# Optimization experiments

Hardware: AMD Instinct MI355X
Metric: run time of the kernel (lower is better)

Reference implementation:

```python
import jax, jax.numpy as jnp
import numpy as np

NUM_CLASS = 80
S = 76              # output_size = 608 // 8 (scale i=0)
STRIDE = 8.0
XYSCALE = 1.2
IOU_LOSS_THRESH = 0.5
INPUT_SIZE = 608.0  # stride * output_size
ANCHORS0 = np.array([[12., 16.], [19., 36.], [40., 28.]], dtype=np.float32)


def setup_inputs() -> dict:
    key = jax.random.key(0)
    k1, k2, k3 = jax.random.split(key, 3)
    B, MAXGT = 16, 150
    conv = jax.random.normal(k1, (B, S, S, 3 * (5 + NUM_CLASS)), dtype=jnp.float32)
    label = jax.random.uniform(k2, (B, S, S, 3, 5 + NUM_CLASS), dtype=jnp.float32)
    # scale the xywh channels of label to pixel coordinates
    label = label.at[..., :4].multiply(INPUT_SIZE)
    bboxes = jax.random.uniform(k3, (B, MAXGT, 4), dtype=jnp.float32) * INPUT_SIZE
    return {"conv": conv, "label": label, "bboxes": bboxes}


def _bce_with_logits(logits, labels):
    # tf.nn.sigmoid_cross_entropy_with_logits, numerically stable form
    return jnp.maximum(logits, 0.0) - logits * labels + jnp.log1p(jnp.exp(-jnp.abs(logits)))


def _xywh_to_corners(b):
    return jnp.concatenate([b[..., :2] - b[..., 2:] * 0.5,
                            b[..., :2] + b[..., 2:] * 0.5], axis=-1)


def _bbox_iou(boxes1, boxes2):
    area1 = boxes1[..., 2] * boxes1[..., 3]
    area2 = boxes2[..., 2] * boxes2[..., 3]
    b1, b2 = _xywh_to_corners(boxes1), _xywh_to_corners(boxes2)
    lu = jnp.maximum(b1[..., :2], b2[..., :2])
    rd = jnp.minimum(b1[..., 2:], b2[..., 2:])
    inter = jnp.maximum(rd - lu, 0.0)
    inter_area = inter[..., 0] * inter[..., 1]
    union = area1 + area2 - inter_area
    return inter_area / union


def _bbox_giou(boxes1, boxes2):
    area1 = boxes1[..., 2] * boxes1[..., 3]
    area2 = boxes2[..., 2] * boxes2[..., 3]
    b1, b2 = _xywh_to_corners(boxes1), _xywh_to_corners(boxes2)
    lu = jnp.maximum(b1[..., :2], b2[..., :2])
    rd = jnp.minimum(b1[..., 2:], b2[..., 2:])
    inter = jnp.maximum(rd - lu, 0.0)
    inter_area = inter[..., 0] * inter[..., 1]
    union = area1 + area2 - inter_area
    iou = inter_area / union
    enc_lu = jnp.minimum(b1[..., :2], b2[..., :2])
    enc_rd = jnp.maximum(b1[..., 2:], b2[..., 2:])
    enc = jnp.maximum(enc_rd - enc_lu, 0.0)
    enc_area = enc[..., 0] * enc[..., 1]
    return iou - (enc_area - union) / enc_area


def _decode_train(conv):
    B = conv.shape[0]
    conv = conv.reshape(B, S, S, 3, 5 + NUM_CLASS)
    dxdy, dwdh, raw_conf, raw_prob = jnp.split(conv, [2, 4, 5], axis=-1)
    xs, ys = jnp.meshgrid(jnp.arange(S), jnp.arange(S))  # indexing='xy' like tf.meshgrid
    grid = jnp.stack([xs, ys], axis=-1)[None, :, :, None, :].astype(jnp.float32)  # [1,S,S,1,2]
    pred_xy = (jax.nn.sigmoid(dxdy) * XYSCALE - 0.5 * (XYSCALE - 1.0) + grid) * STRIDE
    pred_wh = jnp.exp(dwdh) * ANCHORS0  # [B,S,S,3,2]
    return jnp.concatenate([pred_xy, pred_wh,
                            jax.nn.sigmoid(raw_conf), jax.nn.sigmoid(raw_prob)], axis=-1)


def reference(conv, label, bboxes):
    pred = _decode_train(conv)  # [B,S,S,3,5+C]
    B = conv.shape[0]
    conv5 = conv.reshape(B, S, S, 3, 5 + NUM_CLASS)
    conv_raw_conf = conv5[..., 4:5]
    conv_raw_prob = conv5[..., 5:]

    pred_xywh = pred[..., 0:4]
    pred_conf = pred[..., 4:5]

    label_xywh = label[..., 0:4]
    respond_bbox = label[..., 4:5]
    label_prob = label[..., 5:]

    giou = _bbox_giou(pred_xywh, label_xywh)[..., None]
    bbox_loss_scale = 2.0 - label_xywh[..., 2:3] * label_xywh[..., 3:4] / (INPUT_SIZE ** 2)
    giou_loss = respond_bbox * bbox_loss_scale * (1.0 - giou)

    # pairwise IoU: [B,S,S,3,1,4] vs [B,1,1,1,MAXGT,4] -> [B,S,S,3,MAXGT]
    iou = _bbox_iou(pred_xywh[..., None, :], bboxes[:, None, None, None, :, :])
    max_iou = jnp.max(iou, axis=-1, keepdims=True)
    respond_bgd = (1.0 - respond_bbox) * (max_iou < IOU_LOSS_THRESH).astype(jnp.float32)

    conf_focal = jnp.square(respond_bbox - pred_conf)
    bce_conf = _bce_with_logits(conv_raw_conf, respond_bbox)
    conf_loss = conf_focal * (respond_bbox * bce_conf + respond_bgd * bce_conf)
    prob_loss = respond_bbox * _bce_with_logits(conv_raw_prob, label_prob)

    giou_loss = jnp.mean(jnp.sum(giou_loss, axis=(1, 2, 3, 4)))
    conf_loss = jnp.mean(jnp.sum(conf_loss, axis=(1, 2, 3, 4)))
    prob_loss = jnp.mean(jnp.sum(prob_loss, axis=(1, 2, 3, 4)))
    return jnp.stack([giou_loss, conf_loss, prob_loss])
```

## Files before the change

kernel.cpp:

```cpp
#include <hip/hip_runtime.h>
#include <math.h>

#define S 76
#define A 3
#define CH 85
#define MAXGT 150
#define CPB (S * S * A)
#define FPB (CPB * CH)
#define BATCH 16
#define TILE 64
#define BLK 256
#define N4F (TILE * CH / 4)
#define GX ((CPB + TILE - 1) / TILE)
#define NBLK (GX * BATCH)

__device__ __forceinline__ float frcp(float x) { return __builtin_amdgcn_rcpf(x); }
__device__ __forceinline__ float sigmoidf_(float x) { return frcp(1.f + __expf(-x)); }
__device__ __forceinline__ float bcef(float x, float y) {
    const float t  = __builtin_amdgcn_exp2f(x * 1.44269504f);
    const float lg = __builtin_amdgcn_logf(1.f + t);
    return __builtin_fmaf(0.69314718f, lg, -x * y);
}

__global__ __launch_bounds__(BLK) void yolo_unified_kernel(
    const float* __restrict__ conv, const float* __restrict__ label,
    const float* __restrict__ bboxes, float* __restrict__ part)
{
    __shared__ float  s_ch[TILE][5];
    __shared__ float  s_lh[TILE][5];
    __shared__ float  s_resp[TILE];
    __shared__ float4 s_box[MAXGT];
    __shared__ float  s_ba[MAXGT];
    __shared__ float  sred[3][BLK / 64];

    const int b   = blockIdx.y;
    const int tid = threadIdx.x;
    const int base_cell = blockIdx.x * TILE;
    const int ncells = min(TILE, CPB - base_cell);
    const int n4 = (ncells * CH) >> 2;

    const size_t eb = (size_t)b * FPB + (size_t)base_cell * CH;
    const float*  lbb = label + eb;
    const float4* cv4 = (const float4*)(conv + eb);
    const float4* lb4 = (const float4*)lbb;

    if (tid < MAXGT) {
        const float4 bx = *(const float4*)(bboxes + (size_t)b * (MAXGT * 4) + tid * 4);
        const float hw = bx.z * 0.5f, hh = bx.w * 0.5f;
        s_box[tid] = make_float4(3.f * (bx.x - hw), bx.y - hh, 3.f * (bx.x + hw), bx.y + hh);
        s_ba[tid]  = bx.z * bx.w;
    }
    if (tid < TILE)
        s_resp[tid] = (tid < ncells) ? lbb[(size_t)tid * CH + 4] : 0.f;
    __syncthreads();

    float p_sum = 0.f;
    auto body = [&](int u) {
        const float4 cc = cv4[u];
        const float4 lc = lb4[u];
        const unsigned e0 = 4u * (unsigned)u;
        const unsigned c0 = e0 / 85u;
        const unsigned r0 = e0 - 85u * c0;
        const float rsp = s_resp[c0];
        const float cx[4] = {cc.x, cc.y, cc.z, cc.w};
        const float lx[4] = {lc.x, lc.y, lc.z, lc.w};
        float s = 0.f;
        #pragma unroll
        for (int k = 0; k < 4; ++k) {
            const unsigned rr = r0 + (unsigned)k;
            const float bv = bcef(cx[k], lx[k]);
            s += ((rr - 5u) < 80u) ? bv : 0.f;
            const bool hdr = (rr < 5u) || (rr >= 85u);
            if (hdr) {
                const unsigned cell = (rr < 5u) ? c0 : c0 + 1u;
                const unsigned chn  = (rr < 5u) ? rr : rr - 85u;
                s_ch[cell][chn] = cx[k];
                s_lh[cell][chn] = lx[k];
            }
        }
        p_sum = __builtin_fmaf(rsp, s, p_sum);
    };
    if (n4 == N4F) {
        #pragma unroll
        for (int r = 0; r < N4F / BLK; ++r) body(r * BLK + tid);
        if (tid < (N4F - (N4F / BLK) * BLK)) body((N4F / BLK) * BLK + tid);
    } else {
        for (int u = tid; u < n4; u += BLK) body(u);
    }
    __syncthreads();

    const int c = tid >> 2;
    const int q = tid & 3;
    float g_sum = 0.f, c_sum = 0.f;
    if (c < ncells) {
        const int t   = base_cell + c;
        const int i   = t / (S * A);
        const int rem = t - i * (S * A);
        const int j   = rem / A;
        const int a   = rem - j * A;
        const float aw = (a == 0) ? 12.f : ((a == 1) ? 19.f : 40.f);
        const float ah = (a == 0) ? 16.f : ((a == 1) ? 36.f : 28.f);

        const float dx = s_ch[c][0], dy = s_ch[c][1], dw = s_ch[c][2],
                    dh = s_ch[c][3], rc = s_ch[c][4];
        const float lxc = s_lh[c][0], lyc = s_lh[c][1], lwc = s_lh[c][2],
                    lhc = s_lh[c][3], resp = s_lh[c][4];

        const float px = (sigmoidf_(dx) * 1.2f - 0.1f + (float)j) * 8.f;
        const float py = (sigmoidf_(dy) * 1.2f - 0.1f + (float)i) * 8.f;
        const float pw = __expf(dw) * aw;
        const float ph = __expf(dh) * ah;
        const float pconf = sigmoidf_(rc);

        const float px1 = px - pw * 0.5f, py1 = py - ph * 0.5f;
        const float px2 = px + pw * 0.5f, py2 = py + ph * 0.5f;
        const float areap = pw * ph;

        const float px1_3 = 3.f * px1, px2_3 = 3.f * px2;
        float maxv = -1e30f;
        #pragma unroll 5
        for (int k = q; k < MAXGT; k += 4) {
            const float4 bx = s_box[k];
            const float ba  = s_ba[k];
            const float kiw3 = fmaxf(fminf(px2_3, bx.z) - fmaxf(px1_3, bx.x), 0.f);
            const float kih  = fmaxf(fminf(py2, bx.w) - fmaxf(py1, bx.y), 0.f);
            maxv = fmaxf(maxv, __builtin_fmaf(kiw3, kih, -ba));
        }
        maxv = fmaxf(maxv, __shfl_xor(maxv, 1, 64));
        maxv = fmaxf(maxv, __shfl_xor(maxv, 2, 64));

        if (q == 0) {
            const float lx1 = lxc - lwc * 0.5f, ly1 = lyc - lhc * 0.5f;
            const float lx2 = lxc + lwc * 0.5f, ly2 = lyc + lhc * 0.5f;
            const float areal = lwc * lhc;
            const float iw = fmaxf(fminf(px2, lx2) - fmaxf(px1, lx1), 0.f);
            const float ih = fmaxf(fminf(py2, ly2) - fmaxf(py1, ly1), 0.f);
            const float inter = iw * ih;
            const float uni = areap + areal - inter;
            const float iou = inter * frcp(uni);
            const float ew = fmaxf(fmaxf(px2, lx2) - fminf(px1, lx1), 0.f);
            const float eh = fmaxf(fmaxf(py2, ly2) - fminf(py1, ly1), 0.f);
            const float enc = ew * eh;
            const float giou = iou - (enc - uni) * frcp(enc);
            g_sum = resp * (2.f - areal * (1.f / (608.f * 608.f))) * (1.f - giou);

            const float bgd = (1.f - resp) * ((maxv < areap) ? 1.f : 0.f);
            const float focal = (resp - pconf) * (resp - pconf);
            c_sum = focal * (resp + bgd) * bcef(rc, resp);
        }
    }

    for (int off = 32; off > 0; off >>= 1) {
        g_sum += __shfl_down(g_sum, off, 64);
        c_sum += __shfl_down(c_sum, off, 64);
        p_sum += __shfl_down(p_sum, off, 64);
    }
    const int lane = tid & 63, wv = tid >> 6;
    if (lane == 0) { sred[0][wv] = g_sum; sred[1][wv] = c_sum; sred[2][wv] = p_sum; }
    __syncthreads();
    if (tid == 0) {
        float G = 0.f, C = 0.f, P = 0.f;
        #pragma unroll
        for (int w = 0; w < BLK / 64; ++w) { G += sred[0][w]; C += sred[1][w]; P += sred[2][w]; }
        const int bid = blockIdx.y * gridDim.x + blockIdx.x;
        part[bid * 3 + 0] = G;
        part[bid * 3 + 1] = C;
        part[bid * 3 + 2] = P;
    }
}

__global__ __launch_bounds__(256) void final_reduce(
    const float* __restrict__ part, float* __restrict__ out, int nblocks, float invB)
{
    const int tid = threadIdx.x;
    float g = 0.f, c = 0.f, p = 0.f;
    for (int k = tid; k < nblocks; k += 256) {
        g += part[3 * k + 0];
        c += part[3 * k + 1];
        p += part[3 * k + 2];
    }
    for (int off = 32; off > 0; off >>= 1) {
        g += __shfl_down(g, off, 64);
        c += __shfl_down(c, off, 64);
        p += __shfl_down(p, off, 64);
    }
    __shared__ float sred[3][4];
    const int lane = tid & 63, wv = tid >> 6;
    if (lane == 0) { sred[0][wv] = g; sred[1][wv] = c; sred[2][wv] = p; }
    __syncthreads();
    if (tid == 0) {
        float G = 0.f, C = 0.f, P = 0.f;
        #pragma unroll
        for (int w = 0; w < 4; ++w) { G += sred[0][w]; C += sred[1][w]; P += sred[2][w]; }
        out[0] = G * invB;
        out[1] = C * invB;
        out[2] = P * invB;
    }
}

extern "C" void kernel_launch(void* const* d_in, const int* in_sizes, int n_in,
                              void* d_out, int out_size, void* d_ws, size_t ws_size,
                              hipStream_t stream) {
    const float* conv   = (const float*)d_in[0];
    const float* label  = (const float*)d_in[1];
    const float* bboxes = (const float*)d_in[2];
    float* out  = (float*)d_out;
    float* part = (float*)d_ws;

    dim3 grid(GX, BATCH);
    yolo_unified_kernel<<<grid, BLK, 0, stream>>>(conv, label, bboxes, part);
    final_reduce<<<1, 256, 0, stream>>>(part, out, NBLK, 1.f / (float)BATCH);
}
```

Before: 63.72 us.

## Stream tiles via async global-to-LDS ring buffer with larger per-block tiles

Tiles grow from 64 to 192 cells per block. On full tiles, each wave streams its contiguous slice of conv and label through a 4-deep LDS ring using global_load_lds, with explicit vmcnt waits, to overlap memory latency with the BCE math. The max-IoU scan now runs one thread per cell over all 150 boxes instead of four threads per cell plus shuffles. This trades fewer blocks and a serial IoU loop per thread for better latency hiding, and relies on hand-tuned waitcnt ordering that may be fragile.

```diff
diff --git a/kernel.cpp b/kernel.cpp
--- a/kernel.cpp
+++ b/kernel.cpp
@@ -8,11 +8,16 @@
 #define CPB (S * S * A)
 #define FPB (CPB * CH)
 #define BATCH 16
-#define TILE 64
 #define BLK 256
-#define N4F (TILE * CH / 4)
+#define WPB 4
+#define TILE 192
+#define F4_W 1020
+#define ROUNDS 16
+#define DEPTH 4
 #define GX ((CPB + TILE - 1) / TILE)
 #define NBLK (GX * BATCH)
+
+typedef float fx4 __attribute__((ext_vector_type(4)));
 
 __device__ __forceinline__ float frcp(float x) { return __builtin_amdgcn_rcpf(x); }
 __device__ __forceinline__ float sigmoidf_(float x) { return frcp(1.f + __expf(-x)); }
@@ -22,95 +27,163 @@
     return __builtin_fmaf(0.69314718f, lg, -x * y);
 }
 
+template<int N>
+__device__ __forceinline__ void vmwait() {
+    asm volatile("s_waitcnt vmcnt(%0)" :: "i"(N) : "memory");
+    __builtin_amdgcn_sched_barrier(0);
+}
+__device__ __forceinline__ void gl_lds16(const float* g, void* l) {
+    __builtin_amdgcn_global_load_lds(
+        (const __attribute__((address_space(1))) void*)g,
+        (__attribute__((address_space(3))) void*)l, 16, 0, 0);
+}
+
 __global__ __launch_bounds__(BLK) void yolo_unified_kernel(
     const float* __restrict__ conv, const float* __restrict__ label,
     const float* __restrict__ bboxes, float* __restrict__ part)
 {
-    __shared__ float  s_ch[TILE][5];
-    __shared__ float  s_lh[TILE][5];
-    __shared__ float  s_resp[TILE];
-    __shared__ float4 s_box[MAXGT];
-    __shared__ float  s_ba[MAXGT];
-    __shared__ float  sred[3][BLK / 64];
-
-    const int b   = blockIdx.y;
-    const int tid = threadIdx.x;
-    const int base_cell = blockIdx.x * TILE;
+    __shared__ fx4   ring_c[WPB * DEPTH * 64];
+    __shared__ fx4   ring_l[WPB * DEPTH * 64];
+    __shared__ float s_ch[TILE][5];
+    __shared__ float s_lh[TILE][5];
+    __shared__ float s_resp[TILE];
+    __shared__ fx4   s_box[MAXGT];
+    __shared__ float s_ba[MAXGT];
+    __shared__ float sred[3][WPB];
+
+    const int b    = blockIdx.y;
+    const int tile = blockIdx.x;
+    const int tid  = threadIdx.x;
+    const int w    = tid >> 6;
+    const int lane = tid & 63;
+    const int base_cell = tile * TILE;
     const int ncells = min(TILE, CPB - base_cell);
-    const int n4 = (ncells * CH) >> 2;
 
     const size_t eb = (size_t)b * FPB + (size_t)base_cell * CH;
-    const float*  lbb = label + eb;
-    const float4* cv4 = (const float4*)(conv + eb);
-    const float4* lb4 = (const float4*)lbb;
+    const float* cvb = conv  + eb;
+    const float* lbb = label + eb;
 
     if (tid < MAXGT) {
         const float4 bx = *(const float4*)(bboxes + (size_t)b * (MAXGT * 4) + tid * 4);
         const float hw = bx.z * 0.5f, hh = bx.w * 0.5f;
-        s_box[tid] = make_float4(3.f * (bx.x - hw), bx.y - hh, 3.f * (bx.x + hw), bx.y + hh);
+        fx4 v; v.x = 3.f * (bx.x - hw); v.y = bx.y - hh;
+        v.z = 3.f * (bx.x + hw); v.w = bx.y + hh;
+        s_box[tid] = v;
         s_ba[tid]  = bx.z * bx.w;
     }
-    if (tid < TILE)
-        s_resp[tid] = (tid < ncells) ? lbb[(size_t)tid * CH + 4] : 0.f;
+    for (int c = tid; c < ncells; c += BLK)
+        s_resp[c] = lbb[(size_t)c * CH + 4];
     __syncthreads();
 
     float p_sum = 0.f;
-    auto body = [&](int u) {
-        const float4 cc = cv4[u];
-        const float4 lc = lb4[u];
-        const unsigned e0 = 4u * (unsigned)u;
-        const unsigned c0 = e0 / 85u;
-        const unsigned r0 = e0 - 85u * c0;
-        const float rsp = s_resp[c0];
-        const float cx[4] = {cc.x, cc.y, cc.z, cc.w};
-        const float lx[4] = {lc.x, lc.y, lc.z, lc.w};
-        float s = 0.f;
-        #pragma unroll
-        for (int k = 0; k < 4; ++k) {
-            const unsigned rr = r0 + (unsigned)k;
-            const float bv = bcef(cx[k], lx[k]);
-            s += ((rr - 5u) < 80u) ? bv : 0.f;
-            const bool hdr = (rr < 5u) || (rr >= 85u);
-            if (hdr) {
-                const unsigned cell = (rr < 5u) ? c0 : c0 + 1u;
-                const unsigned chn  = (rr < 5u) ? rr : rr - 85u;
-                s_ch[cell][chn] = cx[k];
-                s_lh[cell][chn] = lx[k];
+
+    if (ncells == TILE) {
+        const float* pc = cvb + ((size_t)w * F4_W + (size_t)lane) * 4;
+        const float* pl = lbb + ((size_t)w * F4_W + (size_t)lane) * 4;
+
+        #define SLOT(R) ((w * DEPTH + ((R) & 3)) * 64)
+        #define ISSUE(R)                                                       \
+            gl_lds16(pc + (size_t)(R) * 256, &ring_c[SLOT(R)]);                \
+            gl_lds16(pl + (size_t)(R) * 256, &ring_l[SLOT(R)]);
+
+        ISSUE(0) ISSUE(1) ISSUE(2) ISSUE(3)
+        fx4 rc[2], rl[2];
+        vmwait<6>();
+        rc[0] = ring_c[SLOT(0) + lane];
+        rl[0] = ring_l[SLOT(0) + lane];
+        __builtin_amdgcn_sched_barrier(0);
+
+        #define STEPX(R, W_)                                                    \
+        {                                                                       \
+            if ((R) + 1 < ROUNDS) {                                             \
+                vmwait<W_>();                                                   \
+                rc[((R) + 1) & 1] = ring_c[SLOT((R) + 1) + lane];               \
+                rl[((R) + 1) & 1] = ring_l[SLOT((R) + 1) + lane];               \
+                __builtin_amdgcn_sched_barrier(0);                              \
+            }                                                                   \
+            if ((R) < ROUNDS - 1 || lane < 60) {                                \
+                const fx4 cc = rc[(R) & 1];                                     \
+                const fx4 lc = rl[(R) & 1];                                     \
+                const unsigned e0 = 4u * (unsigned)(w * F4_W + (R) * 64 + lane);\
+                const unsigned c0 = e0 / 85u;                                   \
+                const unsigned r0 = e0 - 85u * c0;                              \
+                const float rsp = s_resp[c0];                                   \
+                const float cxx[4] = {cc.x, cc.y, cc.z, cc.w};                  \
+                const float lxx[4] = {lc.x, lc.y, lc.z, lc.w};                  \
+                float s_ = 0.f;                                                 \
+                _Pragma("unroll")                                               \
+                for (int k = 0; k < 4; ++k) {                                   \
+                    const unsigned rr = r0 + (unsigned)k;           \
+                    const float bv = bcef(cxx[k], lxx[k]);                      \
+                    s_ += ((rr - 5u) < 80u) ? bv : 0.f;                         \
+                    if (rr < 5u)       { s_ch[c0][rr] = cxx[k];                 \
+                                         s_lh[c0][rr] = lxx[k]; }               \
+                    else if (rr >= 85u){ s_ch[c0 + 1][rr - 85u] = cxx[k];       \
+                                         s_lh[c0 + 1][rr - 85u] = lxx[k]; }     \
+                }                                                               \
+                p_sum = __builtin_fmaf(rsp, s_, p_sum);                         \
+            }                                                                   \
+            if ((R) < ROUNDS - 1) {                                             \
+                asm volatile("s_waitcnt lgkmcnt(0)" ::: "memory");              \
+                __builtin_amdgcn_sched_barrier(0);                              \
+                if ((R) + DEPTH < ROUNDS) { ISSUE((R) + DEPTH) }                \
+            }                                                                   \
+        }
+        STEPX(0, 4)  STEPX(1, 4)  STEPX(2, 4)  STEPX(3, 4)
+        STEPX(4, 4)  STEPX(5, 4)  STEPX(6, 4)  STEPX(7, 4)
+        STEPX(8, 4)  STEPX(9, 4)  STEPX(10, 4) STEPX(11, 4)
+        STEPX(12, 4) STEPX(13, 2) STEPX(14, 0) STEPX(15, 0)
+        #undef STEPX
+        #undef ISSUE
+        #undef SLOT
+    } else {
+        const int n4 = (ncells * CH) >> 2;
+        const fx4* cv4 = (const fx4*)cvb;
+        const fx4* lb4 = (const fx4*)lbb;
+        for (int u = tid; u < n4; u += BLK) {
+            const fx4 cc = cv4[u];
+            const fx4 lc = lb4[u];
+            const unsigned e0 = 4u * (unsigned)u;
+            const unsigned c0 = e0 / 85u;
+            const unsigned r0 = e0 - 85u * c0;
+            const float rsp = s_resp[c0];
+            const float cxx[4] = {cc.x, cc.y, cc.z, cc.w};
+            const float lxx[4] = {lc.x, lc.y, lc.z, lc.w};
+            float s_ = 0.f;
+            #pragma unroll
+            for (int k = 0; k < 4; ++k) {
+                const unsigned rr = r0 + (unsigned)k;
+                const float bv = bcef(cxx[k], lxx[k]);
+                s_ += ((rr - 5u) < 80u) ? bv : 0.f;
+                if (rr < 5u)        { s_ch[c0][rr] = cxx[k];  s_lh[c0][rr] = lxx[k]; }
+                else if (rr >= 85u) { s_ch[c0 + 1][rr - 85u] = cxx[k];
+                                      s_lh[c0 + 1][rr - 85u] = lxx[k]; }
             }
+            p_sum = __builtin_fmaf(rsp, s_, p_sum);
         }
-        p_sum = __builtin_fmaf(rsp, s, p_sum);
-    };
-    if (n4 == N4F) {
-        #pragma unroll
-        for (int r = 0; r < N4F / BLK; ++r) body(r * BLK + tid);
-        if (tid < (N4F - (N4F / BLK) * BLK)) body((N4F / BLK) * BLK + tid);
-    } else {
-        for (int u = tid; u < n4; u += BLK) body(u);
-    }
-    __syncthreads();
-
-    const int c = tid >> 2;
-    const int q = tid & 3;
+    }
+    __syncthreads();
+
     float g_sum = 0.f, c_sum = 0.f;
-    if (c < ncells) {
-        const int t   = base_cell + c;
-        const int i   = t / (S * A);
-        const int rem = t - i * (S * A);
+    if (tid < ncells) {
+        const int t_  = base_cell + tid;
+        const int i   = t_ / (S * A);
+        const int rem = t_ - i * (S * A);
         const int j   = rem / A;
         const int a   = rem - j * A;
         const float aw = (a == 0) ? 12.f : ((a == 1) ? 19.f : 40.f);
         const float ah = (a == 0) ? 16.f : ((a == 1) ? 36.f : 28.f);
 
-        const float dx = s_ch[c][0], dy = s_ch[c][1], dw = s_ch[c][2],
-                    dh = s_ch[c][3], rc = s_ch[c][4];
-        const float lxc = s_lh[c][0], lyc = s_lh[c][1], lwc = s_lh[c][2],
-                    lhc = s_lh[c][3], resp = s_lh[c][4];
+        const float dx = s_ch[tid][0], dy = s_ch[tid][1], dw = s_ch[tid][2],
+                    dh = s_ch[tid][3], rcv = s_ch[tid][4];
+        const float lxc = s_lh[tid][0], lyc = s_lh[tid][1], lwc = s_lh[tid][2],
+                    lhc = s_lh[tid][3], resp = s_lh[tid][4];
 
         const float px = (sigmoidf_(dx) * 1.2f - 0.1f + (float)j) * 8.f;
         const float py = (sigmoidf_(dy) * 1.2f - 0.1f + (float)i) * 8.f;
         const float pw = __expf(dw) * aw;
         const float ph = __expf(dh) * ah;
-        const float pconf = sigmoidf_(rc);
+        const float pconf = sigmoidf_(rcv);
 
         const float px1 = px - pw * 0.5f, py1 = py - ph * 0.5f;
         const float px2 = px + pw * 0.5f, py2 = py + ph * 0.5f;
@@ -119,35 +192,31 @@
         const float px1_3 = 3.f * px1, px2_3 = 3.f * px2;
         float maxv = -1e30f;
         #pragma unroll 5
-        for (int k = q; k < MAXGT; k += 4) {
-            const float4 bx = s_box[k];
+        for (int k = 0; k < MAXGT; ++k) {
+            const fx4 bx = s_box[k];
             const float ba  = s_ba[k];
             const float kiw3 = fmaxf(fminf(px2_3, bx.z) - fmaxf(px1_3, bx.x), 0.f);
             const float kih  = fmaxf(fminf(py2, bx.w) - fmaxf(py1, bx.y), 0.f);
             maxv = fmaxf(maxv, __builtin_fmaf(kiw3, kih, -ba));
         }
-        maxv = fmaxf(maxv, __shfl_xor(maxv, 1, 64));
-        maxv = fmaxf(maxv, __shfl_xor(maxv, 2, 64));
-
-        if (q == 0) {
-            const float lx1 = lxc - lwc * 0.5f, ly1 = lyc - lhc * 0.5f;
-            const float lx2 = lxc + lwc * 0.5f, ly2 = lyc + lhc * 0.5f;
-            const float areal = lwc * lhc;
-            const float iw = fmaxf(fminf(px2, lx2) - fmaxf(px1, lx1), 0.f);
-            const float ih = fmaxf(fminf(py2, ly2) - fmaxf(py1, ly1), 0.f);
-            const float inter = iw * ih;
-            const float uni = areap + areal - inter;
-            const float iou = inter * frcp(uni);
-            const float ew = fmaxf(fmaxf(px2, lx2) - fminf(px1, lx1), 0.f);
-            const float eh = fmaxf(fmaxf(py2, ly2) - fminf(py1, ly1), 0.f);
-            const float enc = ew * eh;
-            const float giou = iou - (enc - uni) * frcp(enc);
-            g_sum = resp * (2.f - areal * (1.f / (608.f * 608.f))) * (1.f - giou);
-
-            const float bgd = (1.f - resp) * ((maxv < areap) ? 1.f : 0.f);
-            const float focal = (resp - pconf) * (resp - pconf);
-            c_sum = focal * (resp + bgd) * bcef(rc, resp);
-        }
+
+        const float lx1 = lxc - lwc * 0.5f, ly1 = lyc - lhc * 0.5f;
+        const float lx2 = lxc + lwc * 0.5f, ly2 = lyc + lhc * 0.5f;
+        const float areal = lwc * lhc;
+        const float iw = fmaxf(fminf(px2, lx2) - fmaxf(px1, lx1), 0.f);
+        const float ih = fmaxf(fminf(py2, ly2) - fmaxf(py1, ly1), 0.f);
+        const float inter = iw * ih;
+        const float uni = areap + areal - inter;
+        const float iou = inter * frcp(uni);
+        const float ew = fmaxf(fmaxf(px2, lx2) - fminf(px1, lx1), 0.f);
+        const float eh = fmaxf(fmaxf(py2, ly2) - fminf(py1, ly1), 0.f);
+        const float enc = ew * eh;
+        const float giou = iou - (enc - uni) * frcp(enc);
+        g_sum = resp * (2.f - areal * (1.f / (608.f * 608.f))) * (1.f - giou);
+
+        const float bgd = (1.f - resp) * ((maxv < areap) ? 1.f : 0.f);
+        const float focal = (resp - pconf) * (resp - pconf);
+        c_sum = focal * (resp + bgd) * bcef(rcv, resp);
     }
 
     for (int off = 32; off > 0; off >>= 1) {
@@ -155,13 +224,12 @@
         c_sum += __shfl_down(c_sum, off, 64);
         p_sum += __shfl_down(p_sum, off, 64);
     }
-    const int lane = tid & 63, wv = tid >> 6;
-    if (lane == 0) { sred[0][wv] = g_sum; sred[1][wv] = c_sum; sred[2][wv] = p_sum; }
+    if (lane == 0) { sred[0][w] = g_sum; sred[1][w] = c_sum; sred[2][w] = p_sum; }
     __syncthreads();
     if (tid == 0) {
         float G = 0.f, C = 0.f, P = 0.f;
         #pragma unroll
-        for (int w = 0; w < BLK / 64; ++w) { G += sred[0][w]; C += sred[1][w]; P += sred[2][w]; }
+        for (int q = 0; q < WPB; ++q) { G += sred[0][q]; C += sred[1][q]; P += sred[2][q]; }
         const int bid = blockIdx.y * gridDim.x + blockIdx.x;
         part[bid * 3 + 0] = G;
         part[bid * 3 + 1] = C;
@@ -191,7 +259,7 @@
     if (tid == 0) {
         float G = 0.f, C = 0.f, P = 0.f;
         #pragma unroll
-        for (int w = 0; w < 4; ++w) { G += sred[0][w]; C += sred[1][w]; P += sred[2][w]; }
+        for (int q = 0; q < 4; ++q) { G += sred[0][q]; C += sred[1][q]; P += sred[2][q]; }
         out[0] = G * invB;
         out[1] = C * invB;
         out[2] = P * invB;
```

Measured after the change: 81.84 us. 28.4% more time.
